# Kernel tuning notes

Measured on AMD Instinct MI355X. Metric: run time of the kernel, lower is better.

Reference implementation:

```python
import jax, jax.numpy as jnp
import numpy as np

B, L, K, D, S = 8, 1024, 1024, 128, 16  # batch, nodes, eigvecs, d_model(=d_inner), d_state
ABAR_EPS = 1e-3
BN_EPS = 1e-5


def setup_inputs() -> dict:
    key = jax.random.key(0)
    ks = jax.random.split(key, 10)
    x = jax.random.normal(ks[0], (B, L, D), jnp.float32)
    attn_mask = jnp.ones((B, L), jnp.bool_)
    EigVecs = jax.random.normal(ks[1], (B, L, K), jnp.float32)
    EigVals = jax.random.uniform(ks[2], (B, K), jnp.float32)
    # BatchNorm1d (eval mode) params
    bn_gamma = jnp.ones((D,), jnp.float32)
    bn_beta = jnp.zeros((D,), jnp.float32)
    bn_mean = jnp.zeros((D,), jnp.float32)
    bn_var = jnp.ones((D,), jnp.float32)
    # in_proj Linear(D, 2*D)
    W_in = jax.random.normal(ks[3], (D, 2 * D), jnp.float32) / np.float32(np.sqrt(D))
    b_in = jnp.zeros((2 * D,), jnp.float32)
    # SSM params
    log_Delta = np.float32(np.log(1e-3)) + np.float32(np.log(0.1) - np.log(1e-3)) * jax.random.uniform(ks[4], (1, D), jnp.float32)
    Bp = 0.01 * jax.random.normal(ks[5], (1, D, S), jnp.float32)
    Cp = 0.01 * jax.random.normal(ks[6], (1, D, S), jnp.float32)
    log_A_real = jnp.log(0.5 * jnp.ones((D, S), jnp.float32))
    A_imag = jnp.pi * jnp.broadcast_to(jnp.arange(D, dtype=jnp.float32)[:, None], (D, S))
    # out_proj Linear(D, D)
    W_out = jax.random.normal(ks[7], (D, D), jnp.float32) / np.float32(np.sqrt(D))
    b_out = jnp.zeros((D,), jnp.float32)
    return {
        "x": x, "attn_mask": attn_mask, "EigVecs": EigVecs, "EigVals": EigVals,
        "bn_gamma": bn_gamma, "bn_beta": bn_beta, "bn_mean": bn_mean, "bn_var": bn_var,
        "W_in": W_in, "b_in": b_in, "log_Delta": log_Delta, "Bp": Bp, "Cp": Cp,
        "log_A_real": log_A_real, "A_imag": A_imag, "W_out": W_out, "b_out": b_out,
    }


def reference(x, attn_mask, EigVecs, EigVals, bn_gamma, bn_beta, bn_mean, bn_var,
              W_in, b_in, log_Delta, Bp, Cp, log_A_real, A_imag, W_out, b_out):
    # --- eig preprocessing ---
    ev = 1.0 - EigVals[:, :, None, None]            # (B,K,1,1)
    ev = jnp.nan_to_num(ev)
    Q = jnp.nan_to_num(EigVecs)                      # (B,L,K)
    Q = Q / jnp.linalg.norm(Q, axis=-1, keepdims=True)
    Q = jnp.nan_to_num(Q)
    # --- in_proj: BatchNorm1d (eval) + Linear ---
    xb = (x - bn_mean) * (bn_gamma / jnp.sqrt(bn_var + BN_EPS)) + bn_beta
    h = xb @ W_in + b_in                             # (B,L,2D)
    x1, z = jnp.split(h, 2, axis=-1)                 # split [d_model, d_model]
    u = x1 * jax.nn.silu(z)                          # (B,L,D)
    # --- discretized SSM params ---
    delta = jnp.exp(log_Delta)                       # (1,D)
    A = -jnp.exp(log_A_real) + 1j * A_imag           # (D,S) complex
    Abar = jnp.exp(-ABAR_EPS + delta[..., None] * A) # (1,D,S) complex
    Bbar = delta[..., None] * Bp                     # (1,D,S)
    # --- graph Fourier transform ---
    QTX = jnp.einsum('blk,bld->bkd', Q, u)           # (B,K,D)
    QTXB = QTX[..., None] * Bbar                     # (B,K,D,S)
    lamA = ev * Abar[:, None]                        # (B,K,D,S) complex
    lamQ = jnp.real(lamA / (1.0 - lamA) * QTXB)      # A_complex & not BC_complex -> .real
    # --- inverse transform + C reduction (fused) ---
    yssm = jnp.einsum('blk,bkds,ds->bld', Q, lamQ, Cp[0])  # (B,L,D)
    y = jax.nn.silu(yssm) @ W_out + b_out
    return y
```

## Files before the change

### kernel.cpp

```cpp
#include <hip/hip_runtime.h>
#include <math.h>

#define B_ 8
#define L_ 1024
#define K_ 1024
#define D_ 128
#define S_ 16
#define DS_ (D_ * S_)
#define KS_ 8
#define CSL_ 128
#define NIT_ 4

typedef short bf16x8 __attribute__((ext_vector_type(8)));
typedef float f32x4 __attribute__((ext_vector_type(4)));
typedef __attribute__((address_space(1))) const unsigned int gu32;
typedef __attribute__((address_space(3))) unsigned int lu32;

__device__ inline unsigned short f2bf(float f) {
    unsigned int u = __float_as_uint(f);
    u = (u + 0x7fffu + ((u >> 16) & 1u)) >> 16;
    return (unsigned short)u;
}
__device__ inline float bf2f(unsigned short h) {
    return __uint_as_float(((unsigned int)h) << 16);
}

__device__ inline size_t bswz(int b, int c, int n) {
    return ((((size_t)b * 32 + (c >> 5)) * 4 + ((c >> 3) & 3)) * 128 + n) * 8;
}

__global__ void k_params(const float* __restrict__ log_Delta,
                         const float* __restrict__ Bp,
                         const float* __restrict__ Cp,
                         const float* __restrict__ log_A_real,
                         const float* __restrict__ A_imag,
                         float* __restrict__ par) {
    int i = blockIdx.x * blockDim.x + threadIdx.x;
    if (i >= DS_) return;
    int d = i >> 4;
    int s = i & 15;
    double delta = exp((double)log_Delta[d]);
    double Are = -exp((double)log_A_real[i]);
    double Aim = (double)A_imag[i];
    double mag = exp(-1e-3 + delta * Are);
    double ang = delta * Aim;
    int o = s * D_ + d;
    par[o]            = (float)(mag * cos(ang));
    par[DS_ + o]      = (float)(mag * sin(ang));
    par[2 * DS_ + o]  = (float)(delta * (double)Bp[i] * (double)Cp[i]);
}

__global__ __launch_bounds__(256) void k_pre(
    const float* __restrict__ E, const float* __restrict__ x,
    const float* __restrict__ g, const float* __restrict__ beta,
    const float* __restrict__ mean, const float* __restrict__ var,
    const float* __restrict__ W_in, const float* __restrict__ b_in,
    float* __restrict__ rn_out,
    unsigned short* __restrict__ uswH, unsigned short* __restrict__ uswL) {
    __shared__ float xb[16][128];
    __shared__ float rsum[16];
    __shared__ float rnS[16];
    int row0 = blockIdx.x * 16;
    int t = threadIdx.x;
    {
        int r = t >> 4, tt = t & 15;
        const float4* Ep = (const float4*)(E + (size_t)(row0 + r) * K_);
        float s = 0.f;
        #pragma unroll
        for (int i = 0; i < 16; ++i) {
            float4 v = Ep[tt + i * 16];
            s += v.x * v.x + v.y * v.y + v.z * v.z + v.w * v.w;
        }
        s += __shfl_xor(s, 8, 64);
        s += __shfl_xor(s, 4, 64);
        s += __shfl_xor(s, 2, 64);
        s += __shfl_xor(s, 1, 64);
        if (tt == 0) rsum[r] = s;
    }
    #pragma unroll
    for (int p = 0; p < 8; ++p) {
        int idx = t + p * 256;
        int dd = idx & 127, r = idx >> 7;
        float sc = g[dd] / sqrtf(var[dd] + 1e-5f);
        xb[r][dd] = (x[(size_t)(row0 + r) * D_ + dd] - mean[dd]) * sc + beta[dd];
    }
    __syncthreads();
    if (t < 16) {
        float rv = 1.0f / sqrtf(rsum[t]);
        rnS[t] = rv;
        rn_out[row0 + t] = rv;
    }
    __syncthreads();
    int j = t & 127, half = t >> 7;
    float acc1[8], acc2[8];
    #pragma unroll
    for (int r = 0; r < 8; ++r) { acc1[r] = 0.f; acc2[r] = 0.f; }
    #pragma unroll 4
    for (int dd = 0; dd < 128; ++dd) {
        float w1 = W_in[dd * 256 + j];
        float w2 = W_in[dd * 256 + 128 + j];
        #pragma unroll
        for (int r = 0; r < 8; ++r) {
            float xv = xb[half * 8 + r][dd];
            acc1[r] = fmaf(xv, w1, acc1[r]);
            acc2[r] = fmaf(xv, w2, acc2[r]);
        }
    }
    float b1 = b_in[j], b2 = b_in[128 + j];
    bf16x8 hv, lv;
    #pragma unroll
    for (int r = 0; r < 8; ++r) {
        int rr = half * 8 + r;
        float x1 = acc1[r] + b1;
        float z  = acc2[r] + b2;
        float sig = 1.0f / (1.0f + __expf(-z));
        float uv = rnS[rr] * x1 * z * sig;
        unsigned short h = f2bf(uv);
        hv[r] = (short)h;
        lv[r] = (short)f2bf(uv - bf2f(h));
    }
    int b = row0 >> 10;
    int l0 = (row0 & 1023) + half * 8;
    size_t off = bswz(b, l0, j);
    *(bf16x8*)&uswH[off] = hv;
    *(bf16x8*)&uswL[off] = lv;
}

template<bool ATRANS>
__global__ __launch_bounds__(256, 4) void k_gemm(
    const float* __restrict__ Asrc,
    const unsigned short* __restrict__ BsrcH,
    const unsigned short* __restrict__ BsrcL,
    float* __restrict__ P) {
    __shared__ unsigned short sAh[64 * 40];
    __shared__ unsigned short sAl[64 * 40];
    __shared__ unsigned short sBh[4224];
    __shared__ unsigned short sBl[4224];
    int bx = blockIdx.x;
    int ks = bx & (KS_ - 1);
    int mt16 = (bx >> 3) & 15;
    int b = bx >> 7;
    int m0 = mt16 * 64;
    int cbase = ks * CSL_;
    const float* Ab = Asrc + (size_t)b * 1024 * 1024;
    int t = threadIdx.x;
    int wave = t >> 6, lane = t & 63;
    int fr = lane & 15, q = lane >> 4;
    int wn = wave * 32;
    int m_, cg_;
    if (ATRANS) { m_ = t & 63; cg_ = t >> 6; }
    else        { m_ = t >> 2; cg_ = t & 3; }
    f32x4 acc[4][2];
    #pragma unroll
    for (int i = 0; i < 4; ++i)
        #pragma unroll
        for (int j = 0; j < 2; ++j) acc[i][j] = (f32x4){0.f, 0.f, 0.f, 0.f};

    float v[8];
    if (ATRANS) {
        #pragma unroll
        for (int i = 0; i < 8; ++i)
            v[i] = Ab[(size_t)(cbase + cg_ * 8 + i) * 1024 + m0 + m_];
    } else {
        *(float4*)&v[0] = *(const float4*)&Ab[(size_t)(m0 + m_) * 1024 + cbase + cg_ * 8];
        *(float4*)&v[4] = *(const float4*)&Ab[(size_t)(m0 + m_) * 1024 + cbase + cg_ * 8 + 4];
    }

    #pragma unroll
    for (int it = 0; it < NIT_; ++it) {
        {
            bf16x8 hv, lv;
            #pragma unroll
            for (int i = 0; i < 8; ++i) {
                unsigned short h = f2bf(v[i]);
                hv[i] = (short)h;
                lv[i] = (short)f2bf(v[i] - bf2f(h));
            }
            int p = (cg_ + (m_ >> 3)) & 3;
            *(bf16x8*)&sAh[m_ * 40 + p * 8] = hv;
            *(bf16x8*)&sAl[m_ * 40 + p * 8] = lv;
        }
        {
            int ct = ks * 4 + it;
            size_t src0 = (((size_t)(b * 32 + ct)) * 4) * 1024;
            #pragma unroll
            for (int j = 0; j < 4; ++j) {
                int s = wave + j * 4;
                int qq = s & 3, nh = (s >> 2) & 1, hl = s >> 3;
                const unsigned short* src =
                    (hl ? BsrcL : BsrcH) + src0 + ((size_t)qq * 128 + nh * 64 + lane) * 8;
                unsigned short* dst =
                    (hl ? sBl : sBh) + qq * 1032 + nh * 512;
                __builtin_amdgcn_global_load_lds((gu32*)src, (lu32*)dst, 16, 0, 0);
            }
        }
        __syncthreads();
        if (it + 1 < NIT_) {
            int cb = cbase + (it + 1) * 32;
            if (ATRANS) {
                #pragma unroll
                for (int i = 0; i < 8; ++i)
                    v[i] = Ab[(size_t)(cb + cg_ * 8 + i) * 1024 + m0 + m_];
            } else {
                *(float4*)&v[0] = *(const float4*)&Ab[(size_t)(m0 + m_) * 1024 + cb + cg_ * 8];
                *(float4*)&v[4] = *(const float4*)&Ab[(size_t)(m0 + m_) * 1024 + cb + cg_ * 8 + 4];
            }
        }
        bf16x8 ah[4], al[4], bh[2], bl[2];
        #pragma unroll
        for (int mt = 0; mt < 4; ++mt) {
            int r = mt * 16 + fr;
            int p = (q + (r >> 3)) & 3;
            int off = r * 40 + p * 8;
            ah[mt] = *(const bf16x8*)&sAh[off];
            al[mt] = *(const bf16x8*)&sAl[off];
        }
        #pragma unroll
        for (int nt = 0; nt < 2; ++nt) {
            int off = q * 1032 + (wn + nt * 16 + fr) * 8;
            bh[nt] = *(const bf16x8*)&sBh[off];
            bl[nt] = *(const bf16x8*)&sBl[off];
        }
        #pragma unroll
        for (int mt = 0; mt < 4; ++mt)
            #pragma unroll
            for (int nt = 0; nt < 2; ++nt) {
                acc[mt][nt] = __builtin_amdgcn_mfma_f32_16x16x32_bf16(
                    ah[mt], bh[nt], acc[mt][nt], 0, 0, 0);
                acc[mt][nt] = __builtin_amdgcn_mfma_f32_16x16x32_bf16(
                    ah[mt], bl[nt], acc[mt][nt], 0, 0, 0);
                acc[mt][nt] = __builtin_amdgcn_mfma_f32_16x16x32_bf16(
                    al[mt], bh[nt], acc[mt][nt], 0, 0, 0);
            }
        __syncthreads();
    }
    float* Pb = P + ((size_t)(ks * B_ + b) * 1024 + m0) * 128;
    #pragma unroll
    for (int mt = 0; mt < 4; ++mt)
        #pragma unroll
        for (int nt = 0; nt < 2; ++nt) {
            int col = wn + nt * 16 + fr;
            #pragma unroll
            for (int r = 0; r < 4; ++r)
                Pb[(size_t)(mt * 16 + q * 4 + r) * 128 + col] = acc[mt][nt][r];
        }
}

__global__ __launch_bounds__(256) void k_gepi(
    const float* __restrict__ P, const float* __restrict__ EigVals,
    const float* __restrict__ par,
    unsigned short* __restrict__ GswH, unsigned short* __restrict__ GswL) {
    __shared__ float parS[3 * DS_];
    __shared__ float Gs[16][132];
    int t = threadIdx.x;
    for (int i = t; i < 3 * DS_; i += 256) parS[i] = par[i];
    __syncthreads();
    int bx = blockIdx.x;
    int kt = bx & 63, b = bx >> 6;
    int k0 = kt * 16;
    #pragma unroll
    for (int sub = 0; sub < 2; ++sub) {
        int k = (t >> 5) + sub * 8;
        int d4 = (t & 31) * 4;
        int row = b * 1024 + k0 + k;
        float4 s = {0.f, 0.f, 0.f, 0.f};
        #pragma unroll
        for (int sl = 0; sl < KS_; ++sl) {
            float4 v = *(const float4*)&P[((size_t)sl * 8192 + row) * 128 + d4];
            s.x += v.x; s.y += v.y; s.z += v.z; s.w += v.w;
        }
        float ev = 1.0f - EigVals[row];
        float qv[4] = {s.x, s.y, s.z, s.w};
        float o[4];
        #pragma unroll
        for (int c = 0; c < 4; ++c) {
            int dd = d4 + c;
            float w = 0.f;
            #pragma unroll
            for (int ss = 0; ss < S_; ++ss) {
                float arp = parS[ss * D_ + dd];
                float aip = parS[DS_ + ss * D_ + dd];
                float cc  = parS[2 * DS_ + ss * D_ + dd];
                float a = ev * arp, bi = ev * aip;
                float oma = 1.0f - a;
                float b2 = bi * bi;
                float num = fmaf(a, oma, -b2);
                float den = fmaf(oma, oma, b2);
                float r = __builtin_amdgcn_rcpf(den);
                r = r * (2.0f - den * r);
                w = fmaf(cc, num * r, w);
            }
            o[c] = qv[c] * w;
        }
        *(float4*)&Gs[k][d4] = (float4){o[0], o[1], o[2], o[3]};
    }
    __syncthreads();
    int d = t >> 1, kc = (t & 1) * 8;
    bf16x8 hv, lv;
    #pragma unroll
    for (int i = 0; i < 8; ++i) {
        float v = Gs[kc + i][d];
        unsigned short h = f2bf(v);
        hv[i] = (short)h;
        lv[i] = (short)f2bf(v - bf2f(h));
    }
    size_t off = bswz(b, k0 + kc, d);
    *(bf16x8*)&GswH[off] = hv;
    *(bf16x8*)&GswL[off] = lv;
}

__global__ __launch_bounds__(256) void k_out(
    const float* __restrict__ P, const float* __restrict__ rn,
    const float* __restrict__ W_out, const float* __restrict__ b_out,
    float* __restrict__ y) {
    __shared__ float Ys[16][128];
    int row0 = blockIdx.x * 16;
    int t = threadIdx.x;
    #pragma unroll
    for (int r = 0; r < 2; ++r) {
        int idx = t + r * 256;
        int rr = idx >> 5, d4 = (idx & 31) * 4;
        int grow = row0 + rr;
        float4 s = {0.f, 0.f, 0.f, 0.f};
        #pragma unroll
        for (int sl = 0; sl < KS_; ++sl) {
            float4 v = *(const float4*)&P[((size_t)sl * 8192 + grow) * 128 + d4];
            s.x += v.x; s.y += v.y; s.z += v.z; s.w += v.w;
        }
        float rv = rn[grow];
        float o[4] = {s.x * rv, s.y * rv, s.z * rv, s.w * rv};
        #pragma unroll
        for (int c = 0; c < 4; ++c) {
            float sig = 1.0f / (1.0f + __expf(-o[c]));
            Ys[rr][d4 + c] = o[c] * sig;
        }
    }
    __syncthreads();
    int j = t & 127, h = t >> 7;
    float a2[8];
    #pragma unroll
    for (int r = 0; r < 8; ++r) a2[r] = 0.f;
    for (int dd = 0; dd < 128; dd += 4) {
        float w0 = W_out[(dd + 0) * 128 + j];
        float w1 = W_out[(dd + 1) * 128 + j];
        float w2 = W_out[(dd + 2) * 128 + j];
        float w3 = W_out[(dd + 3) * 128 + j];
        #pragma unroll
        for (int r = 0; r < 8; ++r) {
            float4 yv = *(float4*)&Ys[h * 8 + r][dd];
            a2[r] = fmaf(yv.x, w0, a2[r]);
            a2[r] = fmaf(yv.y, w1, a2[r]);
            a2[r] = fmaf(yv.z, w2, a2[r]);
            a2[r] = fmaf(yv.w, w3, a2[r]);
        }
    }
    float bo = b_out[j];
    #pragma unroll
    for (int r = 0; r < 8; ++r)
        y[(size_t)(row0 + h * 8 + r) * D_ + j] = a2[r] + bo;
}

extern "C" void kernel_launch(void* const* d_in, const int* in_sizes, int n_in,
                              void* d_out, int out_size, void* d_ws, size_t ws_size,
                              hipStream_t stream) {
    const float* x          = (const float*)d_in[0];
    const float* EigVecs    = (const float*)d_in[2];
    const float* EigVals    = (const float*)d_in[3];
    const float* bn_gamma   = (const float*)d_in[4];
    const float* bn_beta    = (const float*)d_in[5];
    const float* bn_mean    = (const float*)d_in[6];
    const float* bn_var     = (const float*)d_in[7];
    const float* W_in       = (const float*)d_in[8];
    const float* b_in       = (const float*)d_in[9];
    const float* log_Delta  = (const float*)d_in[10];
    const float* Bp         = (const float*)d_in[11];
    const float* Cp         = (const float*)d_in[12];
    const float* log_A_real = (const float*)d_in[13];
    const float* A_imag     = (const float*)d_in[14];
    const float* W_out      = (const float*)d_in[15];
    const float* b_out      = (const float*)d_in[16];

    float* y = (float*)d_out;
    char* w = (char*)d_ws;
    float* rn            = (float*)(w);
    float* par           = (float*)(w + 32768);
    unsigned short* uswH = (unsigned short*)(w + 65536);
    unsigned short* uswL = (unsigned short*)(w + 65536 + (1u << 21));
    unsigned short* GswH = (unsigned short*)(w + 65536 + 2 * (1u << 21));
    unsigned short* GswL = (unsigned short*)(w + 65536 + 3 * (1u << 21));
    float* P             = (float*)(w + 65536 + 4 * (1u << 21));

    k_params<<<dim3(8), dim3(256), 0, stream>>>(log_Delta, Bp, Cp, log_A_real, A_imag, par);
    k_pre<<<dim3(B_ * L_ / 16), dim3(256), 0, stream>>>(
        EigVecs, x, bn_gamma, bn_beta, bn_mean, bn_var, W_in, b_in, rn, uswH, uswL);
    k_gemm<true><<<dim3(KS_ * 16 * B_), dim3(256), 0, stream>>>(EigVecs, uswH, uswL, P);
    k_gepi<<<dim3(B_ * 64), dim3(256), 0, stream>>>(P, EigVals, par, GswH, GswL);
    k_gemm<false><<<dim3(KS_ * 16 * B_), dim3(256), 0, stream>>>(EigVecs, GswH, GswL, P);
    k_out<<<dim3(B_ * L_ / 16), dim3(256), 0, stream>>>(P, rn, W_out, b_out, y);
}
```

Measured before the change: 177.1 us.

## Drop split-K GEMMs, fuse SSM epilogue and output projection into GEMM kernels

The two split-K GEMMs (8 K-slices writing fp32 partials) are replaced by full-K GEMMs with 32-row tiles and a double-buffered LDS pipeline. The spectral SSM weighting and bf16 hi/lo packing now run in the first GEMM's epilogue, and the row-norm scale, SiLU and output projection run in the second GEMM's epilogue. The parameter kernel is folded into the first blocks of k_pre. Together this removes the partial-sum buffer traffic and three launches. The cost is only 256 blocks, each running a long serial K loop, which may underfill the GPU.

```diff
diff --git a/kernel.cpp b/kernel.cpp
--- a/kernel.cpp
+++ b/kernel.cpp
@@ -7,9 +7,7 @@
 #define D_ 128
 #define S_ 16
 #define DS_ (D_ * S_)
-#define KS_ 8
-#define CSL_ 128
-#define NIT_ 4
+#define NIT_ 32
 
 typedef short bf16x8 __attribute__((ext_vector_type(8)));
 typedef float f32x4 __attribute__((ext_vector_type(4)));
@@ -27,27 +25,6 @@
 
 __device__ inline size_t bswz(int b, int c, int n) {
     return ((((size_t)b * 32 + (c >> 5)) * 4 + ((c >> 3) & 3)) * 128 + n) * 8;
-}
-
-__global__ void k_params(const float* __restrict__ log_Delta,
-                         const float* __restrict__ Bp,
-                         const float* __restrict__ Cp,
-                         const float* __restrict__ log_A_real,
-                         const float* __restrict__ A_imag,
-                         float* __restrict__ par) {
-    int i = blockIdx.x * blockDim.x + threadIdx.x;
-    if (i >= DS_) return;
-    int d = i >> 4;
-    int s = i & 15;
-    double delta = exp((double)log_Delta[d]);
-    double Are = -exp((double)log_A_real[i]);
-    double Aim = (double)A_imag[i];
-    double mag = exp(-1e-3 + delta * Are);
-    double ang = delta * Aim;
-    int o = s * D_ + d;
-    par[o]            = (float)(mag * cos(ang));
-    par[DS_ + o]      = (float)(mag * sin(ang));
-    par[2 * DS_ + o]  = (float)(delta * (double)Bp[i] * (double)Cp[i]);
 }
 
 __global__ __launch_bounds__(256) void k_pre(
@@ -55,13 +32,30 @@
     const float* __restrict__ g, const float* __restrict__ beta,
     const float* __restrict__ mean, const float* __restrict__ var,
     const float* __restrict__ W_in, const float* __restrict__ b_in,
-    float* __restrict__ rn_out,
+    const float* __restrict__ log_Delta, const float* __restrict__ Bp,
+    const float* __restrict__ Cp, const float* __restrict__ log_A_real,
+    const float* __restrict__ A_imag,
+    float* __restrict__ rn_out, float* __restrict__ par,
     unsigned short* __restrict__ uswH, unsigned short* __restrict__ uswL) {
     __shared__ float xb[16][128];
     __shared__ float rsum[16];
     __shared__ float rnS[16];
-    int row0 = blockIdx.x * 16;
+    int bx = blockIdx.x;
+    int row0 = bx * 16;
     int t = threadIdx.x;
+    if (bx < 8) {
+        int i = bx * 256 + t;
+        int d = i >> 4, s = i & 15;
+        double delta = exp((double)log_Delta[d]);
+        double Are = -exp((double)log_A_real[i]);
+        double Aim = (double)A_imag[i];
+        double mag = exp(-1e-3 + delta * Are);
+        double ang = delta * Aim;
+        int o = s * D_ + d;
+        par[o]           = (float)(mag * cos(ang));
+        par[DS_ + o]     = (float)(mag * sin(ang));
+        par[2 * DS_ + o] = (float)(delta * (double)Bp[i] * (double)Cp[i]);
+    }
     {
         int r = t >> 4, tt = t & 15;
         const float4* Ep = (const float4*)(E + (size_t)(row0 + r) * K_);
@@ -126,103 +120,106 @@
     *(bf16x8*)&uswL[off] = lv;
 }
 
-template<bool ATRANS>
-__global__ __launch_bounds__(256, 4) void k_gemm(
-    const float* __restrict__ Asrc,
-    const unsigned short* __restrict__ BsrcH,
-    const unsigned short* __restrict__ BsrcL,
-    float* __restrict__ P) {
-    __shared__ unsigned short sAh[64 * 40];
-    __shared__ unsigned short sAl[64 * 40];
-    __shared__ unsigned short sBh[4224];
-    __shared__ unsigned short sBl[4224];
+__device__ inline void cvt4_write(const float* v, unsigned short* sh,
+                                  unsigned short* sl, int offShorts) {
+    unsigned short hs[4], ls[4];
+    #pragma unroll
+    for (int i = 0; i < 4; ++i) {
+        hs[i] = f2bf(v[i]);
+        ls[i] = f2bf(v[i] - bf2f(hs[i]));
+    }
+    *(uint2*)&sh[offShorts] = (uint2){(unsigned)hs[0] | ((unsigned)hs[1] << 16),
+                                      (unsigned)hs[2] | ((unsigned)hs[3] << 16)};
+    *(uint2*)&sl[offShorts] = (uint2){(unsigned)ls[0] | ((unsigned)ls[1] << 16),
+                                      (unsigned)ls[2] | ((unsigned)ls[3] << 16)};
+}
+
+__global__ __launch_bounds__(256) void k_g1(
+    const float* __restrict__ E,
+    const unsigned short* __restrict__ BH, const unsigned short* __restrict__ BL,
+    const float* __restrict__ EigVals, const float* __restrict__ par,
+    unsigned short* __restrict__ GswH, unsigned short* __restrict__ GswL) {
+    __shared__ unsigned short sAh[2][1280], sAl[2][1280];
+    __shared__ unsigned short sBh[2][4128], sBl[2][4128];
+    __shared__ float evS[32];
+    __shared__ float Gs[32][132];
     int bx = blockIdx.x;
-    int ks = bx & (KS_ - 1);
-    int mt16 = (bx >> 3) & 15;
-    int b = bx >> 7;
-    int m0 = mt16 * 64;
-    int cbase = ks * CSL_;
-    const float* Ab = Asrc + (size_t)b * 1024 * 1024;
+    int b = bx & 7;
+    int m0 = (bx >> 3) * 32;
+    const float* Ab = E + (size_t)b * (1024 * 1024);
+    const unsigned short* BbH = BH + (size_t)b * 131072;
+    const unsigned short* BbL = BL + (size_t)b * 131072;
     int t = threadIdx.x;
     int wave = t >> 6, lane = t & 63;
     int fr = lane & 15, q = lane >> 4;
     int wn = wave * 32;
-    int m_, cg_;
-    if (ATRANS) { m_ = t & 63; cg_ = t >> 6; }
-    else        { m_ = t >> 2; cg_ = t & 3; }
-    f32x4 acc[4][2];
-    #pragma unroll
-    for (int i = 0; i < 4; ++i)
-        #pragma unroll
-        for (int j = 0; j < 2; ++j) acc[i][j] = (f32x4){0.f, 0.f, 0.f, 0.f};
-
-    float v[8];
-    if (ATRANS) {
-        #pragma unroll
-        for (int i = 0; i < 8; ++i)
-            v[i] = Ab[(size_t)(cbase + cg_ * 8 + i) * 1024 + m0 + m_];
-    } else {
-        *(float4*)&v[0] = *(const float4*)&Ab[(size_t)(m0 + m_) * 1024 + cbase + cg_ * 8];
-        *(float4*)&v[4] = *(const float4*)&Ab[(size_t)(m0 + m_) * 1024 + cbase + cg_ * 8 + 4];
-    }
-
-    #pragma unroll
+    int am = t & 31, acg = t >> 5;
+    int ap = ((acg >> 1) + (am >> 3)) & 3;
+    int aoff = am * 40 + ap * 8 + (acg & 1) * 4;
+    if (t < 32) evS[t] = 1.0f - EigVals[b * 1024 + m0 + t];
+    f32x4 acc[2][2];
+    #pragma unroll
+    for (int i = 0; i < 2; ++i)
+        #pragma unroll
+        for (int jj = 0; jj < 2; ++jj) acc[i][jj] = (f32x4){0.f, 0.f, 0.f, 0.f};
+    float va[2][4];
+    {
+        #pragma unroll
+        for (int i = 0; i < 4; ++i)
+            va[0][i] = Ab[(size_t)(acg * 4 + i) * 1024 + m0 + am];
+        size_t src0 = 0;
+        #pragma unroll
+        for (int jj = 0; jj < 4; ++jj) {
+            int s = wave + jj * 4;
+            int qq = s & 3, nh = (s >> 2) & 1, hl = s >> 3;
+            const unsigned short* src =
+                (hl ? BbL : BbH) + src0 + ((size_t)qq * 128 + nh * 64 + lane) * 8;
+            unsigned short* dst = (hl ? sBl[0] : sBh[0]) + qq * 1032 + nh * 512;
+            __builtin_amdgcn_global_load_lds((gu32*)src, (lu32*)dst, 16, 0, 0);
+        }
+        cvt4_write(va[0], sAh[0], sAl[0], aoff);
+        #pragma unroll
+        for (int i = 0; i < 4; ++i)
+            va[1][i] = Ab[(size_t)(32 + acg * 4 + i) * 1024 + m0 + am];
+    }
+    __syncthreads();
     for (int it = 0; it < NIT_; ++it) {
-        {
-            bf16x8 hv, lv;
-            #pragma unroll
-            for (int i = 0; i < 8; ++i) {
-                unsigned short h = f2bf(v[i]);
-                hv[i] = (short)h;
-                lv[i] = (short)f2bf(v[i] - bf2f(h));
-            }
-            int p = (cg_ + (m_ >> 3)) & 3;
-            *(bf16x8*)&sAh[m_ * 40 + p * 8] = hv;
-            *(bf16x8*)&sAl[m_ * 40 + p * 8] = lv;
-        }
-        {
-            int ct = ks * 4 + it;
-            size_t src0 = (((size_t)(b * 32 + ct)) * 4) * 1024;
-            #pragma unroll
-            for (int j = 0; j < 4; ++j) {
-                int s = wave + j * 4;
+        int cur = it & 1, nxt = cur ^ 1;
+        if (it + 1 < NIT_) {
+            size_t src0 = (size_t)(it + 1) * 4096;
+            #pragma unroll
+            for (int jj = 0; jj < 4; ++jj) {
+                int s = wave + jj * 4;
                 int qq = s & 3, nh = (s >> 2) & 1, hl = s >> 3;
                 const unsigned short* src =
-                    (hl ? BsrcL : BsrcH) + src0 + ((size_t)qq * 128 + nh * 64 + lane) * 8;
-                unsigned short* dst =
-                    (hl ? sBl : sBh) + qq * 1032 + nh * 512;
+                    (hl ? BbL : BbH) + src0 + ((size_t)qq * 128 + nh * 64 + lane) * 8;
+                unsigned short* dst = (hl ? sBl[nxt] : sBh[nxt]) + qq * 1032 + nh * 512;
                 __builtin_amdgcn_global_load_lds((gu32*)src, (lu32*)dst, 16, 0, 0);
             }
-        }
-        __syncthreads();
-        if (it + 1 < NIT_) {
-            int cb = cbase + (it + 1) * 32;
-            if (ATRANS) {
-                #pragma unroll
-                for (int i = 0; i < 8; ++i)
-                    v[i] = Ab[(size_t)(cb + cg_ * 8 + i) * 1024 + m0 + m_];
-            } else {
-                *(float4*)&v[0] = *(const float4*)&Ab[(size_t)(m0 + m_) * 1024 + cb + cg_ * 8];
-                *(float4*)&v[4] = *(const float4*)&Ab[(size_t)(m0 + m_) * 1024 + cb + cg_ * 8 + 4];
-            }
-        }
-        bf16x8 ah[4], al[4], bh[2], bl[2];
-        #pragma unroll
-        for (int mt = 0; mt < 4; ++mt) {
+            cvt4_write(va[(it + 1) & 1], sAh[nxt], sAl[nxt], aoff);
+        }
+        if (it + 2 < NIT_) {
+            #pragma unroll
+            for (int i = 0; i < 4; ++i)
+                va[it & 1][i] = Ab[(size_t)((it + 2) * 32 + acg * 4 + i) * 1024 + m0 + am];
+        }
+        bf16x8 ah[2], al[2], bh[2], bl[2];
+        #pragma unroll
+        for (int mt = 0; mt < 2; ++mt) {
             int r = mt * 16 + fr;
             int p = (q + (r >> 3)) & 3;
             int off = r * 40 + p * 8;
-            ah[mt] = *(const bf16x8*)&sAh[off];
-            al[mt] = *(const bf16x8*)&sAl[off];
+            ah[mt] = *(const bf16x8*)&sAh[cur][off];
+            al[mt] = *(const bf16x8*)&sAl[cur][off];
         }
         #pragma unroll
         for (int nt = 0; nt < 2; ++nt) {
             int off = q * 1032 + (wn + nt * 16 + fr) * 8;
-            bh[nt] = *(const bf16x8*)&sBh[off];
-            bl[nt] = *(const bf16x8*)&sBl[off];
-        }
-        #pragma unroll
-        for (int mt = 0; mt < 4; ++mt)
+            bh[nt] = *(const bf16x8*)&sBh[cur][off];
+            bl[nt] = *(const bf16x8*)&sBl[cur][off];
+        }
+        #pragma unroll
+        for (int mt = 0; mt < 2; ++mt)
             #pragma unroll
             for (int nt = 0; nt < 2; ++nt) {
                 acc[mt][nt] = __builtin_amdgcn_mfma_f32_16x16x32_bf16(
@@ -234,120 +231,182 @@
             }
         __syncthreads();
     }
-    float* Pb = P + ((size_t)(ks * B_ + b) * 1024 + m0) * 128;
-    #pragma unroll
-    for (int mt = 0; mt < 4; ++mt)
+    #pragma unroll
+    for (int mt = 0; mt < 2; ++mt)
         #pragma unroll
         for (int nt = 0; nt < 2; ++nt) {
             int col = wn + nt * 16 + fr;
             #pragma unroll
             for (int r = 0; r < 4; ++r)
-                Pb[(size_t)(mt * 16 + q * 4 + r) * 128 + col] = acc[mt][nt][r];
-        }
-}
-
-__global__ __launch_bounds__(256) void k_gepi(
-    const float* __restrict__ P, const float* __restrict__ EigVals,
-    const float* __restrict__ par,
-    unsigned short* __restrict__ GswH, unsigned short* __restrict__ GswL) {
-    __shared__ float parS[3 * DS_];
-    __shared__ float Gs[16][132];
-    int t = threadIdx.x;
-    for (int i = t; i < 3 * DS_; i += 256) parS[i] = par[i];
-    __syncthreads();
-    int bx = blockIdx.x;
-    int kt = bx & 63, b = bx >> 6;
-    int k0 = kt * 16;
-    #pragma unroll
-    for (int sub = 0; sub < 2; ++sub) {
-        int k = (t >> 5) + sub * 8;
-        int d4 = (t & 31) * 4;
-        int row = b * 1024 + k0 + k;
-        float4 s = {0.f, 0.f, 0.f, 0.f};
-        #pragma unroll
-        for (int sl = 0; sl < KS_; ++sl) {
-            float4 v = *(const float4*)&P[((size_t)sl * 8192 + row) * 128 + d4];
-            s.x += v.x; s.y += v.y; s.z += v.z; s.w += v.w;
-        }
-        float ev = 1.0f - EigVals[row];
-        float qv[4] = {s.x, s.y, s.z, s.w};
-        float o[4];
-        #pragma unroll
-        for (int c = 0; c < 4; ++c) {
-            int dd = d4 + c;
+                Gs[mt * 16 + q * 4 + r][col] = acc[mt][nt][r];
+        }
+    __syncthreads();
+    {
+        int col = t & 127, rowg = t >> 7;
+        float arr[S_], aii[S_], ccc[S_];
+        #pragma unroll
+        for (int ss = 0; ss < S_; ++ss) {
+            arr[ss] = par[ss * D_ + col];
+            aii[ss] = par[DS_ + ss * D_ + col];
+            ccc[ss] = par[2 * DS_ + ss * D_ + col];
+        }
+        #pragma unroll
+        for (int i = 0; i < 16; ++i) {
+            int row = rowg * 16 + i;
+            float ev = evS[row];
             float w = 0.f;
             #pragma unroll
             for (int ss = 0; ss < S_; ++ss) {
-                float arp = parS[ss * D_ + dd];
-                float aip = parS[DS_ + ss * D_ + dd];
-                float cc  = parS[2 * DS_ + ss * D_ + dd];
-                float a = ev * arp, bi = ev * aip;
+                float a = ev * arr[ss], bi = ev * aii[ss];
                 float oma = 1.0f - a;
                 float b2 = bi * bi;
                 float num = fmaf(a, oma, -b2);
                 float den = fmaf(oma, oma, b2);
-                float r = __builtin_amdgcn_rcpf(den);
-                r = r * (2.0f - den * r);
-                w = fmaf(cc, num * r, w);
-            }
-            o[c] = qv[c] * w;
-        }
-        *(float4*)&Gs[k][d4] = (float4){o[0], o[1], o[2], o[3]};
-    }
-    __syncthreads();
-    int d = t >> 1, kc = (t & 1) * 8;
-    bf16x8 hv, lv;
-    #pragma unroll
-    for (int i = 0; i < 8; ++i) {
-        float v = Gs[kc + i][d];
-        unsigned short h = f2bf(v);
-        hv[i] = (short)h;
-        lv[i] = (short)f2bf(v - bf2f(h));
-    }
-    size_t off = bswz(b, k0 + kc, d);
-    *(bf16x8*)&GswH[off] = hv;
-    *(bf16x8*)&GswL[off] = lv;
-}
-
-__global__ __launch_bounds__(256) void k_out(
-    const float* __restrict__ P, const float* __restrict__ rn,
-    const float* __restrict__ W_out, const float* __restrict__ b_out,
-    float* __restrict__ y) {
-    __shared__ float Ys[16][128];
-    int row0 = blockIdx.x * 16;
+                float rr = __builtin_amdgcn_rcpf(den);
+                rr = rr * (2.0f - den * rr);
+                w = fmaf(ccc[ss], num * rr, w);
+            }
+            Gs[row][col] *= w;
+        }
+    }
+    __syncthreads();
+    int ct = m0 >> 5;
+    #pragma unroll
+    for (int jj = 0; jj < 2; ++jj) {
+        int tau = t + jj * 256;
+        int d = tau & 127, kg = tau >> 7;
+        bf16x8 hv, lv;
+        #pragma unroll
+        for (int i = 0; i < 8; ++i) {
+            float v = Gs[kg * 8 + i][d];
+            unsigned short h = f2bf(v);
+            hv[i] = (short)h;
+            lv[i] = (short)f2bf(v - bf2f(h));
+        }
+        size_t off = (((size_t)(b * 32 + ct) * 4 + kg) * 128 + d) * 8;
+        *(bf16x8*)&GswH[off] = hv;
+        *(bf16x8*)&GswL[off] = lv;
+    }
+}
+
+__global__ __launch_bounds__(256) void k_g2(
+    const float* __restrict__ E,
+    const unsigned short* __restrict__ BH, const unsigned short* __restrict__ BL,
+    const float* __restrict__ rn, const float* __restrict__ W_out,
+    const float* __restrict__ b_out, float* __restrict__ y) {
+    __shared__ unsigned short sAh[2][1280], sAl[2][1280];
+    __shared__ unsigned short sBh[2][4128], sBl[2][4128];
+    __shared__ float Ys[32][132];
+    __shared__ float rnS[32];
+    int bx = blockIdx.x;
+    int b = bx & 7;
+    int m0 = (bx >> 3) * 32;
+    const float* Ab = E + (size_t)b * (1024 * 1024);
+    const unsigned short* BbH = BH + (size_t)b * 131072;
+    const unsigned short* BbL = BL + (size_t)b * 131072;
     int t = threadIdx.x;
-    #pragma unroll
-    for (int r = 0; r < 2; ++r) {
-        int idx = t + r * 256;
-        int rr = idx >> 5, d4 = (idx & 31) * 4;
-        int grow = row0 + rr;
-        float4 s = {0.f, 0.f, 0.f, 0.f};
-        #pragma unroll
-        for (int sl = 0; sl < KS_; ++sl) {
-            float4 v = *(const float4*)&P[((size_t)sl * 8192 + grow) * 128 + d4];
-            s.x += v.x; s.y += v.y; s.z += v.z; s.w += v.w;
-        }
-        float rv = rn[grow];
-        float o[4] = {s.x * rv, s.y * rv, s.z * rv, s.w * rv};
-        #pragma unroll
-        for (int c = 0; c < 4; ++c) {
-            float sig = 1.0f / (1.0f + __expf(-o[c]));
-            Ys[rr][d4 + c] = o[c] * sig;
-        }
-    }
+    int wave = t >> 6, lane = t & 63;
+    int fr = lane & 15, q = lane >> 4;
+    int wn = wave * 32;
+    int am = t >> 3, acg = t & 7;
+    int ap = ((acg >> 1) + (am >> 3)) & 3;
+    int aoff = am * 40 + ap * 8 + (acg & 1) * 4;
+    if (t < 32) rnS[t] = rn[b * 1024 + m0 + t];
+    f32x4 acc[2][2];
+    #pragma unroll
+    for (int i = 0; i < 2; ++i)
+        #pragma unroll
+        for (int jj = 0; jj < 2; ++jj) acc[i][jj] = (f32x4){0.f, 0.f, 0.f, 0.f};
+    float va[2][4];
+    {
+        *(float4*)&va[0][0] = *(const float4*)&Ab[(size_t)(m0 + am) * 1024 + acg * 4];
+        size_t src0 = 0;
+        #pragma unroll
+        for (int jj = 0; jj < 4; ++jj) {
+            int s = wave + jj * 4;
+            int qq = s & 3, nh = (s >> 2) & 1, hl = s >> 3;
+            const unsigned short* src =
+                (hl ? BbL : BbH) + src0 + ((size_t)qq * 128 + nh * 64 + lane) * 8;
+            unsigned short* dst = (hl ? sBl[0] : sBh[0]) + qq * 1032 + nh * 512;
+            __builtin_amdgcn_global_load_lds((gu32*)src, (lu32*)dst, 16, 0, 0);
+        }
+        cvt4_write(va[0], sAh[0], sAl[0], aoff);
+        *(float4*)&va[1][0] = *(const float4*)&Ab[(size_t)(m0 + am) * 1024 + 32 + acg * 4];
+    }
+    __syncthreads();
+    for (int it = 0; it < NIT_; ++it) {
+        int cur = it & 1, nxt = cur ^ 1;
+        if (it + 1 < NIT_) {
+            size_t src0 = (size_t)(it + 1) * 4096;
+            #pragma unroll
+            for (int jj = 0; jj < 4; ++jj) {
+                int s = wave + jj * 4;
+                int qq = s & 3, nh = (s >> 2) & 1, hl = s >> 3;
+                const unsigned short* src =
+                    (hl ? BbL : BbH) + src0 + ((size_t)qq * 128 + nh * 64 + lane) * 8;
+                unsigned short* dst = (hl ? sBl[nxt] : sBh[nxt]) + qq * 1032 + nh * 512;
+                __builtin_amdgcn_global_load_lds((gu32*)src, (lu32*)dst, 16, 0, 0);
+            }
+            cvt4_write(va[(it + 1) & 1], sAh[nxt], sAl[nxt], aoff);
+        }
+        if (it + 2 < NIT_) {
+            *(float4*)&va[it & 1][0] =
+                *(const float4*)&Ab[(size_t)(m0 + am) * 1024 + (it + 2) * 32 + acg * 4];
+        }
+        bf16x8 ah[2], al[2], bh[2], bl[2];
+        #pragma unroll
+        for (int mt = 0; mt < 2; ++mt) {
+            int r = mt * 16 + fr;
+            int p = (q + (r >> 3)) & 3;
+            int off = r * 40 + p * 8;
+            ah[mt] = *(const bf16x8*)&sAh[cur][off];
+            al[mt] = *(const bf16x8*)&sAl[cur][off];
+        }
+        #pragma unroll
+        for (int nt = 0; nt < 2; ++nt) {
+            int off = q * 1032 + (wn + nt * 16 + fr) * 8;
+            bh[nt] = *(const bf16x8*)&sBh[cur][off];
+            bl[nt] = *(const bf16x8*)&sBl[cur][off];
+        }
+        #pragma unroll
+        for (int mt = 0; mt < 2; ++mt)
+            #pragma unroll
+            for (int nt = 0; nt < 2; ++nt) {
+                acc[mt][nt] = __builtin_amdgcn_mfma_f32_16x16x32_bf16(
+                    ah[mt], bh[nt], acc[mt][nt], 0, 0, 0);
+                acc[mt][nt] = __builtin_amdgcn_mfma_f32_16x16x32_bf16(
+                    ah[mt], bl[nt], acc[mt][nt], 0, 0, 0);
+                acc[mt][nt] = __builtin_amdgcn_mfma_f32_16x16x32_bf16(
+                    al[mt], bh[nt], acc[mt][nt], 0, 0, 0);
+            }
+        __syncthreads();
+    }
+    #pragma unroll
+    for (int mt = 0; mt < 2; ++mt)
+        #pragma unroll
+        for (int nt = 0; nt < 2; ++nt) {
+            int col = wn + nt * 16 + fr;
+            #pragma unroll
+            for (int r = 0; r < 4; ++r) {
+                int row = mt * 16 + q * 4 + r;
+                float v = acc[mt][nt][r] * rnS[row];
+                float sig = 1.0f / (1.0f + __expf(-v));
+                Ys[row][col] = v * sig;
+            }
+        }
     __syncthreads();
     int j = t & 127, h = t >> 7;
-    float a2[8];
-    #pragma unroll
-    for (int r = 0; r < 8; ++r) a2[r] = 0.f;
+    float a2[16];
+    #pragma unroll
+    for (int r = 0; r < 16; ++r) a2[r] = 0.f;
     for (int dd = 0; dd < 128; dd += 4) {
         float w0 = W_out[(dd + 0) * 128 + j];
         float w1 = W_out[(dd + 1) * 128 + j];
         float w2 = W_out[(dd + 2) * 128 + j];
         float w3 = W_out[(dd + 3) * 128 + j];
         #pragma unroll
-        for (int r = 0; r < 8; ++r) {
-            float4 yv = *(float4*)&Ys[h * 8 + r][dd];
+        for (int r = 0; r < 16; ++r) {
+            float4 yv = *(float4*)&Ys[h * 16 + r][dd];
             a2[r] = fmaf(yv.x, w0, a2[r]);
             a2[r] = fmaf(yv.y, w1, a2[r]);
             a2[r] = fmaf(yv.z, w2, a2[r]);
@@ -356,8 +415,8 @@
     }
     float bo = b_out[j];
     #pragma unroll
-    for (int r = 0; r < 8; ++r)
-        y[(size_t)(row0 + h * 8 + r) * D_ + j] = a2[r] + bo;
+    for (int r = 0; r < 16; ++r)
+        y[((size_t)b * 1024 + m0 + h * 16 + r) * 128 + j] = a2[r] + bo;
 }
 
 extern "C" void kernel_launch(void* const* d_in, const int* in_sizes, int n_in,
@@ -388,13 +447,12 @@
     unsigned short* uswL = (unsigned short*)(w + 65536 + (1u << 21));
     unsigned short* GswH = (unsigned short*)(w + 65536 + 2 * (1u << 21));
     unsigned short* GswL = (unsigned short*)(w + 65536 + 3 * (1u << 21));
-    float* P             = (float*)(w + 65536 + 4 * (1u << 21));
-
-    k_params<<<dim3(8), dim3(256), 0, stream>>>(log_Delta, Bp, Cp, log_A_real, A_imag, par);
+
     k_pre<<<dim3(B_ * L_ / 16), dim3(256), 0, stream>>>(
-        EigVecs, x, bn_gamma, bn_beta, bn_mean, bn_var, W_in, b_in, rn, uswH, uswL);
-    k_gemm<true><<<dim3(KS_ * 16 * B_), dim3(256), 0, stream>>>(EigVecs, uswH, uswL, P);
-    k_gepi<<<dim3(B_ * 64), dim3(256), 0, stream>>>(P, EigVals, par, GswH, GswL);
-    k_gemm<false><<<dim3(KS_ * 16 * B_), dim3(256), 0, stream>>>(EigVecs, GswH, GswL, P);
-    k_out<<<dim3(B_ * L_ / 16), dim3(256), 0, stream>>>(P, rn, W_out, b_out, y);
-}
+        EigVecs, x, bn_gamma, bn_beta, bn_mean, bn_var, W_in, b_in,
+        log_Delta, Bp, Cp, log_A_real, A_imag, rn, par, uswH, uswL);
+    k_g1<<<dim3(256), dim3(256), 0, stream>>>(
+        EigVecs, uswH, uswL, EigVals, par, GswH, GswL);
+    k_g2<<<dim3(256), dim3(256), 0, stream>>>(
+        EigVecs, GswH, GswL, rn, W_out, b_out, y);
+}
```

Result: slower. 220.3 us (+24.4%).
